# Optimization experiments

Hardware: AMD Instinct MI355X
Metric: run time of the kernel (lower is better)

Reference implementation:

```python
import jax, jax.numpy as jnp
import numpy as np

DIM = 192
HEADS = 6
WS = (4, 8, 8)  # window size (D, H, W)
N = WS[0] * WS[1] * WS[2]  # 256 tokens per window
NW = 64
B_ = 256  # batch * nW


def _relative_position_index(ws):
    d, h, w = ws
    coords = jnp.stack(jnp.meshgrid(jnp.arange(d), jnp.arange(h), jnp.arange(w), indexing='ij'))
    coords = coords.reshape(3, -1)  # (3, N)
    rel = coords[:, :, None] - coords[:, None, :]  # (3, N, N)
    rel = rel.transpose(1, 2, 0) + jnp.array([d - 1, h - 1, w - 1])
    idx = rel[..., 0] * ((2 * h - 1) * (2 * w - 1)) + rel[..., 1] * (2 * w - 1) + rel[..., 2]
    return idx.astype(jnp.int32)  # (N, N)


def setup_inputs() -> dict:
    key = jax.random.key(0)
    ks = jax.random.split(key, 7)
    table_rows = (2 * WS[0] - 1) * (2 * WS[1] - 1) * (2 * WS[2] - 1)  # 1575
    return {
        'x': jax.random.normal(ks[0], (B_, N, DIM), dtype=jnp.float32),
        'mask': jax.random.normal(ks[1], (NW, N, N), dtype=jnp.float32),
        'qkv_w': jax.random.normal(ks[2], (DIM, 3 * DIM), dtype=jnp.float32) * 0.02,
        'qkv_b': jnp.zeros((3 * DIM,), dtype=jnp.float32),
        'proj_w': jax.random.normal(ks[3], (DIM, DIM), dtype=jnp.float32) * 0.02,
        'proj_b': jnp.zeros((DIM,), dtype=jnp.float32),
        'bias_table': jax.random.normal(ks[4], (table_rows, HEADS), dtype=jnp.float32) * 0.02,
        'rel_index': _relative_position_index(WS),
    }


def reference(x, mask, qkv_w, qkv_b, proj_w, proj_b, bias_table, rel_index):
    B, Ntok, C = x.shape
    hd = C // HEADS
    scale = hd ** (-0.5)
    qkv = (x @ qkv_w + qkv_b).reshape(B, Ntok, 3, HEADS, hd)
    qkv = qkv.transpose(2, 0, 3, 1, 4)  # (3, B, H, N, hd)
    q, k, v = qkv[0], qkv[1], qkv[2]
    attn = jnp.einsum('bhnd,bhmd->bhnm', q * scale, k)  # (B, H, N, N)
    # gathered relative-position bias: (N, N, H) -> (H, N, N)
    bias = bias_table[rel_index.reshape(-1)].reshape(Ntok, Ntok, HEADS).transpose(2, 0, 1)
    attn = attn + bias[None]
    nW = mask.shape[0]
    attn = attn.reshape(B // nW, nW, HEADS, Ntok, Ntok) + mask[None, :, None]
    attn = attn.reshape(B, HEADS, Ntok, Ntok)
    attn = jax.nn.softmax(attn, axis=-1)
    out = jnp.einsum('bhnm,bhmd->bhnd', attn, v)  # (B, H, N, hd)
    out = out.transpose(0, 2, 1, 3).reshape(B, Ntok, C)
    out = out @ proj_w + proj_b
    return out
```

## Files before the change

kernel.cpp:

```cpp
#include <hip/hip_runtime.h>
#include <cstdint>
#include <math.h>

#define DIMC 192
#define NTOK 256
#define HEADS 6
#define HD 32
#define L2E 1.4426950408889634f

typedef __bf16 bf16x8 __attribute__((ext_vector_type(8)));
typedef __bf16 bf16x4 __attribute__((ext_vector_type(4)));
typedef float f32x4 __attribute__((ext_vector_type(4)));

__device__ __forceinline__ void gload_lds16(const __bf16* g, __bf16* l) {
    __builtin_amdgcn_global_load_lds((const __attribute__((address_space(1))) void*)g,
                                     (__attribute__((address_space(3))) void*)l, 16, 0, 0);
}

__global__ void prep(const float* __restrict__ x, __bf16* __restrict__ xb,
                     const float* __restrict__ qkv_w, __bf16* __restrict__ wqt,
                     const float* __restrict__ proj_w, __bf16* __restrict__ wpt,
                     const float* __restrict__ table, const int* __restrict__ rel,
                     __bf16* __restrict__ biasb) {
    const int bid = blockIdx.x, t = threadIdx.x;
    if (bid < 6144) {
        int i = bid * 256 + t;
        float4 a = ((const float4*)x)[i * 2];
        float4 b = ((const float4*)x)[i * 2 + 1];
        bf16x8 o = {(__bf16)a.x, (__bf16)a.y, (__bf16)a.z, (__bf16)a.w,
                    (__bf16)b.x, (__bf16)b.y, (__bf16)b.z, (__bf16)b.w};
        ((bf16x8*)xb)[i] = o;
    } else if (bid < 6576) {
        int i = (bid - 6144) * 256 + t;
        int n = i / DIMC, k = i - n * DIMC;
        wqt[i] = (__bf16)qkv_w[(size_t)k * 576 + n];
    } else if (bid < 6720) {
        int i = (bid - 6576) * 256 + t;
        int n = i / DIMC, k = i - n * DIMC;
        wpt[i] = (__bf16)proj_w[(size_t)k * DIMC + n];
    } else {
        int i = (bid - 6720) * 256 + t;
        int h = i >> 16;
        int r = i & 65535;
        biasb[i] = (__bf16)(table[rel[r] * 6 + h] * L2E);
    }
}

__launch_bounds__(256, 2)
__global__ void qkvbm(const __bf16* __restrict__ A, const __bf16* __restrict__ Wt,
                      const float* __restrict__ bias,
                      __bf16* __restrict__ qo, __bf16* __restrict__ ko, __bf16* __restrict__ vo,
                      const float* __restrict__ mask, const __bf16* __restrict__ biasb,
                      __bf16* __restrict__ bm) {
    __shared__ __bf16 As[256 * 64];
    __shared__ __bf16 Bs[96 * 64];
    const int t = threadIdx.x;
    const int lin = blockIdx.x;

    if (lin >= 1536) {
        int i = (lin - 1536) * 256 + t;
        int w = i >> 13, oct = i & 8191;
        float4 m0 = ((const float4*)mask)[(size_t)w * 16384 + oct * 2];
        float4 m1 = ((const float4*)mask)[(size_t)w * 16384 + oct * 2 + 1];
        #pragma unroll
        for (int h = 0; h < 6; ++h) {
            bf16x8 bb = ((const bf16x8*)biasb)[h * 8192 + oct];
            bf16x8 o = {(__bf16)(m0.x * L2E + (float)bb[0]), (__bf16)(m0.y * L2E + (float)bb[1]),
                        (__bf16)(m0.z * L2E + (float)bb[2]), (__bf16)(m0.w * L2E + (float)bb[3]),
                        (__bf16)(m1.x * L2E + (float)bb[4]), (__bf16)(m1.y * L2E + (float)bb[5]),
                        (__bf16)(m1.z * L2E + (float)bb[6]), (__bf16)(m1.w * L2E + (float)bb[7])};
            ((bf16x8*)bm)[(size_t)(w * 6 + h) * 8192 + oct] = o;
        }
        return;
    }

    const int wv = t >> 6, lane = t & 63;
    const int l16 = lane & 15, quad = lane >> 4;
    const int xcd = lin & 7, pos = lin >> 3;
    const int bx = pos % 6;
    const int by = xcd + (pos / 6) * 8;
    const int m0 = by * 256;
    const int j0 = bx * 96;

    f32x4 acc[4][6];
    #pragma unroll
    for (int mt = 0; mt < 4; ++mt)
        #pragma unroll
        for (int nt = 0; nt < 6; ++nt)
            acc[mt][nt] = (f32x4){0.f, 0.f, 0.f, 0.f};

    for (int kit = 0; kit < 3; ++kit) {
        const int k0 = kit * 64;
        #pragma unroll
        for (int gi = 0; gi < 8; ++gi) {
            int g = wv * 8 + gi;
            int cid = g * 64 + lane;
            int row = cid >> 3, kcs = cid & 7;
            int kcg = kcs ^ (row & 7);
            gload_lds16(A + (size_t)(m0 + row) * DIMC + k0 + kcg * 8, As + g * 512);
        }
        #pragma unroll
        for (int gi = 0; gi < 3; ++gi) {
            int g = wv * 3 + gi;
            int cid = g * 64 + lane;
            int n = cid >> 3, kcs = cid & 7;
            int kcg = kcs ^ (n & 7);
            gload_lds16(Wt + (size_t)(j0 + n) * DIMC + k0 + kcg * 8, Bs + g * 512);
        }
        __syncthreads();
        #pragma unroll
        for (int kk = 0; kk < 2; ++kk) {
            bf16x8 af[4], bfr[6];
            #pragma unroll
            for (int mt = 0; mt < 4; ++mt) {
                int row = wv * 64 + mt * 16 + l16;
                int ch = (kk * 4 + quad) ^ (row & 7);
                af[mt] = *(const bf16x8*)(As + row * 64 + ch * 8);
            }
            #pragma unroll
            for (int nt = 0; nt < 6; ++nt) {
                int n = nt * 16 + l16;
                int ch = (kk * 4 + quad) ^ (n & 7);
                bfr[nt] = *(const bf16x8*)(Bs + n * 64 + ch * 8);
            }
            #pragma unroll
            for (int mt = 0; mt < 4; ++mt)
                #pragma unroll
                for (int nt = 0; nt < 6; ++nt)
                    acc[mt][nt] = __builtin_amdgcn_mfma_f32_16x16x32_bf16(af[mt], bfr[nt], acc[mt][nt], 0, 0, 0);
        }
        __syncthreads();
    }

    const int which = bx >> 1;
    __bf16* outp = which == 0 ? qo : (which == 1 ? ko : vo);
    const float sc = which == 0 ? (0.17677669529663687f * L2E) : 1.0f;
    float bq[6];
    #pragma unroll
    for (int nt = 0; nt < 6; ++nt) bq[nt] = bias[j0 + nt * 16 + l16];
    const int cloc = (bx & 1) * 96;
    __bf16* tile = As + wv * 4096;
    const int TP = 104;
    #pragma unroll
    for (int mt = 0; mt < 4; ++mt) {
        #pragma unroll
        for (int nt = 0; nt < 6; ++nt)
            #pragma unroll
            for (int r = 0; r < 4; ++r)
                tile[(quad * 4 + r) * TP + nt * 16 + l16] = (__bf16)((acc[mt][nt][r] + bq[nt]) * sc);
        int row = lane >> 2;
        #pragma unroll
        for (int it = 0; it < 3; ++it) {
            int c8 = (lane & 3) + it * 4;
            bf16x8 val = *(const bf16x8*)(tile + row * TP + c8 * 8);
            int token = m0 + wv * 64 + mt * 16 + row;
            int b = token >> 8, n = token & 255;
            int cw = cloc + c8 * 8;
            int h = cw >> 5, d0 = cw & 31;
            *(bf16x8*)(outp + (((size_t)b * HEADS + h) * NTOK + n) * HD + d0) = val;
        }
    }
}

__launch_bounds__(256, 3)
__global__ void attn_mfma(const __bf16* __restrict__ qg, const __bf16* __restrict__ kg,
                          const __bf16* __restrict__ vg, const __bf16* __restrict__ bm,
                          __bf16* __restrict__ aout) {
    __shared__ __bf16 Ks[NTOK][40];
    __shared__ __bf16 VTs[HD][264];
    __shared__ __bf16 Ps[4][16][40];
    __shared__ float  Sums[4][64];

    const int lin = blockIdx.x;
    const int xcd = lin & 7, pos = lin >> 3;
    const int g = xcd + (pos >> 2) * 8;
    const int i4 = pos & 3;
    const int h = g % 6, w = g / 6;
    const int b = i4 * 64 + w;
    const int bh = b * HEADS + h;

    const int t = threadIdx.x;
    const size_t base = (size_t)bh * (NTOK * HD);

    #pragma unroll
    for (int it = 0; it < 4; ++it) {
        int c = t + 256 * it;
        int row = c >> 2, off = c & 3;
        *(uint4*)(&Ks[row][off * 8]) = *(const uint4*)(kg + base + row * HD + off * 8);
    }
    #pragma unroll
    for (int it = 0; it < 4; ++it) {
        int d0 = it * 8;
        bf16x8 vv = *(const bf16x8*)(vg + base + t * HD + d0);
        #pragma unroll
        for (int j = 0; j < 8; ++j)
            VTs[d0 + j][t] = vv[j];
    }
    __syncthreads();

    const int wv = t >> 6, lane = t & 63;
    const int l16 = lane & 15, quad = lane >> 4;
    const int q0 = wv * 64;

    bf16x8 qf[4];
    #pragma unroll
    for (int qt = 0; qt < 4; ++qt)
        qf[qt] = *(const bf16x8*)(qg + base + (size_t)(q0 + qt * 16 + l16) * HD + quad * 8);

    f32x4 o[4][2];
    #pragma unroll
    for (int qt = 0; qt < 4; ++qt)
        #pragma unroll
        for (int dt = 0; dt < 2; ++dt)
            o[qt][dt] = (f32x4){0.f, 0.f, 0.f, 0.f};
    float rsum[4] = {};

    const __bf16* bmq = bm + (size_t)(w * 6 + h) * 65536 + (size_t)(q0 + l16) * 256 + quad * 4;

    bf16x4 bmv[4][2];
    #pragma unroll
    for (int qt = 0; qt < 4; ++qt)
        #pragma unroll
        for (int kt = 0; kt < 2; ++kt)
            bmv[qt][kt] = *(const bf16x4*)(bmq + qt * 4096 + kt * 16);

    for (int c = 0; c < 8; ++c) {
        const int kb = c * 32;
        bf16x4 bmn[4][2];
        if (c < 7) {
            #pragma unroll
            for (int qt = 0; qt < 4; ++qt)
                #pragma unroll
                for (int kt = 0; kt < 2; ++kt)
                    bmn[qt][kt] = *(const bf16x4*)(bmq + qt * 4096 + kb + 32 + kt * 16);
        }
        bf16x8 kf[2];
        #pragma unroll
        for (int kt = 0; kt < 2; ++kt)
            kf[kt] = *(const bf16x8*)(&Ks[kb + kt * 16 + l16][quad * 8]);
        bf16x8 vf[2];
        #pragma unroll
        for (int dt = 0; dt < 2; ++dt)
            vf[dt] = *(const bf16x8*)(&VTs[dt * 16 + l16][kb + quad * 8]);

        #pragma unroll
        for (int qt = 0; qt < 4; ++qt) {
            #pragma unroll
            for (int kt = 0; kt < 2; ++kt) {
                f32x4 s = (f32x4){0.f, 0.f, 0.f, 0.f};
                s = __builtin_amdgcn_mfma_f32_16x16x32_bf16(kf[kt], qf[qt], s, 0, 0, 0);
                bf16x4 pk;
                #pragma unroll
                for (int r = 0; r < 4; ++r) {
                    float p = __builtin_amdgcn_exp2f(s[r] + (float)bmv[qt][kt][r]);
                    rsum[qt] += p;
                    pk[r] = (__bf16)p;
                }
                *(bf16x4*)(&Ps[wv][l16][kt * 16 + quad * 4]) = pk;
            }
            bf16x8 pf = *(const bf16x8*)(&Ps[wv][l16][quad * 8]);
            #pragma unroll
            for (int dt = 0; dt < 2; ++dt)
                o[qt][dt] = __builtin_amdgcn_mfma_f32_16x16x32_bf16(pf, vf[dt], o[qt][dt], 0, 0, 0);
        }
        if (c < 7) {
            #pragma unroll
            for (int qt = 0; qt < 4; ++qt)
                #pragma unroll
                for (int kt = 0; kt < 2; ++kt)
                    bmv[qt][kt] = bmn[qt][kt];
        }
    }

    #pragma unroll
    for (int qt = 0; qt < 4; ++qt) {
        float s = rsum[qt];
        s += __shfl_xor(s, 16);
        s += __shfl_xor(s, 32);
        if (quad == 0) Sums[wv][qt * 16 + l16] = 1.0f / s;
    }
    #pragma unroll
    for (int qt = 0; qt < 4; ++qt) {
        f32x4 inv = *(const f32x4*)(&Sums[wv][qt * 16 + quad * 4]);
        #pragma unroll
        for (int dt = 0; dt < 2; ++dt)
            #pragma unroll
            for (int r = 0; r < 4; ++r) {
                int qrow = q0 + qt * 16 + quad * 4 + r;
                aout[((size_t)b * NTOK + qrow) * DIMC + h * HD + dt * 16 + l16] =
                    (__bf16)(o[qt][dt][r] * inv[r]);
            }
    }
}

__launch_bounds__(256, 2)
__global__ void proj_mfma(const __bf16* __restrict__ A, const __bf16* __restrict__ Wt,
                          const float* __restrict__ bias, float* __restrict__ out) {
    __shared__ __bf16 As[256 * 64];
    __shared__ __bf16 Bs[96 * 64];
    const int t = threadIdx.x;
    const int wv = t >> 6, lane = t & 63;
    const int l16 = lane & 15, quad = lane >> 4;

    const int lin = blockIdx.x + blockIdx.y * 2;
    const int xcd = lin & 7, pos = lin >> 3;
    const int bx = pos & 1;
    const int by = xcd + (pos >> 1) * 8;

    const int m0 = by * 256;
    const int j0 = bx * 96;

    f32x4 acc[4][6];
    #pragma unroll
    for (int mt = 0; mt < 4; ++mt)
        #pragma unroll
        for (int nt = 0; nt < 6; ++nt)
            acc[mt][nt] = (f32x4){0.f, 0.f, 0.f, 0.f};

    for (int kit = 0; kit < 3; ++kit) {
        const int k0 = kit * 64;
        #pragma unroll
        for (int gi = 0; gi < 8; ++gi) {
            int g = wv * 8 + gi;
            int cid = g * 64 + lane;
            int row = cid >> 3, kcs = cid & 7;
            int kcg = kcs ^ (row & 7);
            gload_lds16(A + (size_t)(m0 + row) * DIMC + k0 + kcg * 8, As + g * 512);
        }
        #pragma unroll
        for (int gi = 0; gi < 3; ++gi) {
            int g = wv * 3 + gi;
            int cid = g * 64 + lane;
            int n = cid >> 3, kcs = cid & 7;
            int kcg = kcs ^ (n & 7);
            gload_lds16(Wt + (size_t)(j0 + n) * DIMC + k0 + kcg * 8, Bs + g * 512);
        }
        __syncthreads();
        #pragma unroll
        for (int kk = 0; kk < 2; ++kk) {
            bf16x8 af[4], bfr[6];
            #pragma unroll
            for (int mt = 0; mt < 4; ++mt) {
                int row = wv * 64 + mt * 16 + l16;
                int ch = (kk * 4 + quad) ^ (row & 7);
                af[mt] = *(const bf16x8*)(As + row * 64 + ch * 8);
            }
            #pragma unroll
            for (int nt = 0; nt < 6; ++nt) {
                int n = nt * 16 + l16;
                int ch = (kk * 4 + quad) ^ (n & 7);
                bfr[nt] = *(const bf16x8*)(Bs + n * 64 + ch * 8);
            }
            #pragma unroll
            for (int mt = 0; mt < 4; ++mt)
                #pragma unroll
                for (int nt = 0; nt < 6; ++nt)
                    acc[mt][nt] = __builtin_amdgcn_mfma_f32_16x16x32_bf16(af[mt], bfr[nt], acc[mt][nt], 0, 0, 0);
        }
        __syncthreads();
    }

    #pragma unroll
    for (int nt = 0; nt < 6; ++nt) {
        int colg = j0 + nt * 16 + l16;
        float bv = bias[colg];
        #pragma unroll
        for (int mt = 0; mt < 4; ++mt)
            #pragma unroll
            for (int r = 0; r < 4; ++r) {
                int token = m0 + wv * 64 + mt * 16 + quad * 4 + r;
                out[(size_t)token * DIMC + colg] = acc[mt][nt][r] + bv;
            }
    }
}

extern "C" void kernel_launch(void* const* d_in, const int* in_sizes, int n_in,
                              void* d_out, int out_size, void* d_ws, size_t ws_size,
                              hipStream_t stream) {
    const float* x          = (const float*)d_in[0];
    const float* mask       = (const float*)d_in[1];
    const float* qkv_w      = (const float*)d_in[2];
    const float* qkv_b      = (const float*)d_in[3];
    const float* proj_w     = (const float*)d_in[4];
    const float* proj_b     = (const float*)d_in[5];
    const float* bias_table = (const float*)d_in[6];
    const int*   rel_index  = (const int*)d_in[7];

    char* ws = (char*)d_ws;
    __bf16* xb    = (__bf16*)(ws);
    __bf16* q     = (__bf16*)(ws + 25165824);
    __bf16* k     = (__bf16*)(ws + 50331648);
    __bf16* v     = (__bf16*)(ws + 75497472);
    __bf16* biasb = (__bf16*)(ws + 100663296);
    __bf16* wqt   = (__bf16*)(ws + 102236160);
    __bf16* wpt   = (__bf16*)(ws + 102457344);
    __bf16* aoutb = xb;
    __bf16* bm    = (__bf16*)d_out;

    prep<<<8256, 256, 0, stream>>>(x, xb, qkv_w, wqt, proj_w, wpt, bias_table, rel_index, biasb);
    qkvbm<<<3584, 256, 0, stream>>>(xb, wqt, qkv_b, q, k, v, mask, biasb, bm);
    attn_mfma<<<1536, 256, 0, stream>>>(q, k, v, bm, aoutb);
    proj_mfma<<<dim3(2, 256), 256, 0, stream>>>(aoutb, wpt, proj_b, (float*)d_out);
}
```

Measured before the change: 221.4 us.

## Write V transposed from QKV kernel and read K/V directly from global in attention

The QKV projection kernel now stores V in a transposed (d-major) layout, and the attention kernel reads K and V fragments straight from global memory instead of staging them through LDS with a transposing copy and block barrier. With the LDS footprint reduced, the launch bound rises from 3 to 4 blocks per SM. Bias-mask prefetch is dropped in favour of loading it per chunk. This trades LDS traffic and a sync for redundant global/L2 reads across the four waves, with some risk of higher memory latency exposure.

```diff
diff --git a/kernel.cpp b/kernel.cpp
--- a/kernel.cpp
+++ b/kernel.cpp
@@ -139,35 +139,56 @@
     #pragma unroll
     for (int nt = 0; nt < 6; ++nt) bq[nt] = bias[j0 + nt * 16 + l16];
     const int cloc = (bx & 1) * 96;
-    __bf16* tile = As + wv * 4096;
-    const int TP = 104;
-    #pragma unroll
-    for (int mt = 0; mt < 4; ++mt) {
-        #pragma unroll
-        for (int nt = 0; nt < 6; ++nt)
-            #pragma unroll
-            for (int r = 0; r < 4; ++r)
-                tile[(quad * 4 + r) * TP + nt * 16 + l16] = (__bf16)((acc[mt][nt][r] + bq[nt]) * sc);
-        int row = lane >> 2;
-        #pragma unroll
-        for (int it = 0; it < 3; ++it) {
-            int c8 = (lane & 3) + it * 4;
-            bf16x8 val = *(const bf16x8*)(tile + row * TP + c8 * 8);
-            int token = m0 + wv * 64 + mt * 16 + row;
-            int b = token >> 8, n = token & 255;
-            int cw = cloc + c8 * 8;
-            int h = cw >> 5, d0 = cw & 31;
-            *(bf16x8*)(outp + (((size_t)b * HEADS + h) * NTOK + n) * HD + d0) = val;
-        }
-    }
-}
-
-__launch_bounds__(256, 3)
+    const int b = m0 >> 8;
+
+    if (which != 2) {
+        __bf16* tile = As + wv * 4096;
+        const int TP = 104;
+        #pragma unroll
+        for (int mt = 0; mt < 4; ++mt) {
+            #pragma unroll
+            for (int nt = 0; nt < 6; ++nt)
+                #pragma unroll
+                for (int r = 0; r < 4; ++r)
+                    tile[(quad * 4 + r) * TP + nt * 16 + l16] = (__bf16)((acc[mt][nt][r] + bq[nt]) * sc);
+            int row = lane >> 2;
+            #pragma unroll
+            for (int it = 0; it < 3; ++it) {
+                int c8 = (lane & 3) + it * 4;
+                bf16x8 val = *(const bf16x8*)(tile + row * TP + c8 * 8);
+                int n = wv * 64 + mt * 16 + row;
+                int cw = cloc + c8 * 8;
+                int h = cw >> 5, d0 = cw & 31;
+                *(bf16x8*)(outp + (((size_t)b * HEADS + h) * NTOK + n) * HD + d0) = val;
+            }
+        }
+    } else {
+        __bf16* tileT = As + wv * 4096;
+        #pragma unroll
+        for (int mt = 0; mt < 4; ++mt) {
+            #pragma unroll
+            for (int nt = 0; nt < 6; ++nt)
+                #pragma unroll
+                for (int r = 0; r < 4; ++r)
+                    tileT[(nt * 16 + l16) * 16 + quad * 4 + r] = (__bf16)(acc[mt][nt][r] + bq[nt]);
+            int n0 = wv * 64 + mt * 16;
+            #pragma unroll
+            for (int it = 0; it < 3; ++it) {
+                int qid = lane + 64 * it;
+                int col = qid >> 1, half = qid & 1;
+                bf16x8 val = *(const bf16x8*)(tileT + col * 16 + half * 8);
+                int cw = cloc + col;
+                int h = cw >> 5, d = cw & 31;
+                *(bf16x8*)(outp + (((size_t)b * HEADS + h) * HD + d) * NTOK + n0 + half * 8) = val;
+            }
+        }
+    }
+}
+
+__launch_bounds__(256, 4)
 __global__ void attn_mfma(const __bf16* __restrict__ qg, const __bf16* __restrict__ kg,
-                          const __bf16* __restrict__ vg, const __bf16* __restrict__ bm,
+                          const __bf16* __restrict__ vtg, const __bf16* __restrict__ bm,
                           __bf16* __restrict__ aout) {
-    __shared__ __bf16 Ks[NTOK][40];
-    __shared__ __bf16 VTs[HD][264];
     __shared__ __bf16 Ps[4][16][40];
     __shared__ float  Sums[4][64];
 
@@ -180,27 +201,10 @@
     const int bh = b * HEADS + h;
 
     const int t = threadIdx.x;
-    const size_t base = (size_t)bh * (NTOK * HD);
-
-    #pragma unroll
-    for (int it = 0; it < 4; ++it) {
-        int c = t + 256 * it;
-        int row = c >> 2, off = c & 3;
-        *(uint4*)(&Ks[row][off * 8]) = *(const uint4*)(kg + base + row * HD + off * 8);
-    }
-    #pragma unroll
-    for (int it = 0; it < 4; ++it) {
-        int d0 = it * 8;
-        bf16x8 vv = *(const bf16x8*)(vg + base + t * HD + d0);
-        #pragma unroll
-        for (int j = 0; j < 8; ++j)
-            VTs[d0 + j][t] = vv[j];
-    }
-    __syncthreads();
-
     const int wv = t >> 6, lane = t & 63;
     const int l16 = lane & 15, quad = lane >> 4;
     const int q0 = wv * 64;
+    const size_t base = (size_t)bh * (NTOK * HD);
 
     bf16x8 qf[4];
     #pragma unroll
@@ -215,33 +219,31 @@
             o[qt][dt] = (f32x4){0.f, 0.f, 0.f, 0.f};
     float rsum[4] = {};
 
+    const __bf16* kp  = kg  + base + (size_t)l16 * HD + quad * 8;
+    const __bf16* vp  = vtg + base + (size_t)l16 * NTOK + quad * 8;
     const __bf16* bmq = bm + (size_t)(w * 6 + h) * 65536 + (size_t)(q0 + l16) * 256 + quad * 4;
 
-    bf16x4 bmv[4][2];
-    #pragma unroll
-    for (int qt = 0; qt < 4; ++qt)
-        #pragma unroll
-        for (int kt = 0; kt < 2; ++kt)
-            bmv[qt][kt] = *(const bf16x4*)(bmq + qt * 4096 + kt * 16);
+    bf16x8 kf[2];
+    kf[0] = *(const bf16x8*)(kp);
+    kf[1] = *(const bf16x8*)(kp + 16 * HD);
 
     for (int c = 0; c < 8; ++c) {
         const int kb = c * 32;
-        bf16x4 bmn[4][2];
+        bf16x4 bmv[4][2];
+        #pragma unroll
+        for (int qt = 0; qt < 4; ++qt)
+            #pragma unroll
+            for (int kt = 0; kt < 2; ++kt)
+                bmv[qt][kt] = *(const bf16x4*)(bmq + qt * 4096 + kb + kt * 16);
+        bf16x8 vf[2];
+        #pragma unroll
+        for (int dt = 0; dt < 2; ++dt)
+            vf[dt] = *(const bf16x8*)(vp + dt * 16 * NTOK + kb);
+        bf16x8 kfn[2];
         if (c < 7) {
-            #pragma unroll
-            for (int qt = 0; qt < 4; ++qt)
-                #pragma unroll
-                for (int kt = 0; kt < 2; ++kt)
-                    bmn[qt][kt] = *(const bf16x4*)(bmq + qt * 4096 + kb + 32 + kt * 16);
-        }
-        bf16x8 kf[2];
-        #pragma unroll
-        for (int kt = 0; kt < 2; ++kt)
-            kf[kt] = *(const bf16x8*)(&Ks[kb + kt * 16 + l16][quad * 8]);
-        bf16x8 vf[2];
-        #pragma unroll
-        for (int dt = 0; dt < 2; ++dt)
-            vf[dt] = *(const bf16x8*)(&VTs[dt * 16 + l16][kb + quad * 8]);
+            kfn[0] = *(const bf16x8*)(kp + (kb + 32) * HD);
+            kfn[1] = *(const bf16x8*)(kp + (kb + 48) * HD);
+        }
 
         #pragma unroll
         for (int qt = 0; qt < 4; ++qt) {
@@ -263,13 +265,7 @@
             for (int dt = 0; dt < 2; ++dt)
                 o[qt][dt] = __builtin_amdgcn_mfma_f32_16x16x32_bf16(pf, vf[dt], o[qt][dt], 0, 0, 0);
         }
-        if (c < 7) {
-            #pragma unroll
-            for (int qt = 0; qt < 4; ++qt)
-                #pragma unroll
-                for (int kt = 0; kt < 2; ++kt)
-                    bmv[qt][kt] = bmn[qt][kt];
-        }
+        if (c < 7) { kf[0] = kfn[0]; kf[1] = kfn[1]; }
     }
 
     #pragma unroll
@@ -390,7 +386,7 @@
     __bf16* xb    = (__bf16*)(ws);
     __bf16* q     = (__bf16*)(ws + 25165824);
     __bf16* k     = (__bf16*)(ws + 50331648);
-    __bf16* v     = (__bf16*)(ws + 75497472);
+    __bf16* vT    = (__bf16*)(ws + 75497472);
     __bf16* biasb = (__bf16*)(ws + 100663296);
     __bf16* wqt   = (__bf16*)(ws + 102236160);
     __bf16* wpt   = (__bf16*)(ws + 102457344);
@@ -398,7 +394,7 @@
     __bf16* bm    = (__bf16*)d_out;
 
     prep<<<8256, 256, 0, stream>>>(x, xb, qkv_w, wqt, proj_w, wpt, bias_table, rel_index, biasb);
-    qkvbm<<<3584, 256, 0, stream>>>(xb, wqt, qkv_b, q, k, v, mask, biasb, bm);
-    attn_mfma<<<1536, 256, 0, stream>>>(q, k, v, bm, aoutb);
+    qkvbm<<<3584, 256, 0, stream>>>(xb, wqt, qkv_b, q, k, vT, mask, biasb, bm);
+    attn_mfma<<<1536, 256, 0, stream>>>(q, k, vT, bm, aoutb);
     proj_mfma<<<dim3(2, 256), 256, 0, stream>>>(aoutb, wpt, proj_b, (float*)d_out);
 }
```

After: 233.2 us. +5.3%, slower.
